# Optimization experiments

Measured on AMD Instinct MI355X. Metric: run time of the kernel, lower is better.

Reference implementation:

```python
import jax, jax.numpy as jnp
import numpy as np

B, CIN, COUT, H, W = 8, 256, 256, 64, 64
WBIT = 4  # weight_bit


def _fake_quant_sym(w, bits):
    # Symmetric per-tensor fake quantization with straight-through rounding.
    n = 2.0 ** (bits - 1) - 1
    mag = jax.lax.stop_gradient(
        jnp.maximum(jnp.abs(jnp.min(w)), jnp.abs(jnp.max(w))))
    s = jnp.maximum(mag, 1e-8) / n
    q = w / s
    q = q + jax.lax.stop_gradient(jnp.round(q) - q)  # STE round
    return jnp.clip(q, -n - 1, n) * s


def _conv3x3(x, w, b):
    out = jax.lax.conv_general_dilated(
        x, w, window_strides=(1, 1), padding=((1, 1), (1, 1)),
        dimension_numbers=('NCHW', 'OIHW', 'NCHW'))
    return out + b[None, :, None, None]


def _bilinear_gather(x, py, px):
    # x: [B,C,H,W]; py, px: [B,K,Ho,Wo] float sample coords. Zero outside.
    b, c, h, w = x.shape
    y0 = jnp.floor(py)
    x0 = jnp.floor(px)
    wy = (py - y0)[:, None]  # [B,1,K,Ho,Wo]
    wx = (px - x0)[:, None]
    flat = x.reshape(b, c, h * w)

    def gather(yi, xi):
        valid = (yi >= 0) & (yi <= h - 1) & (xi >= 0) & (xi <= w - 1)
        yc = jnp.clip(yi, 0, h - 1).astype(jnp.int32)
        xc = jnp.clip(xi, 0, w - 1).astype(jnp.int32)
        idx = (yc * w + xc).reshape(b, -1)  # [B, K*Ho*Wo]
        g = jax.vmap(lambda f, i: f[:, i])(flat, idx)  # [B,C,K*Ho*Wo]
        g = g.reshape(b, c, *yi.shape[1:])  # [B,C,K,Ho,Wo]
        return g * valid[:, None].astype(x.dtype)

    v00 = gather(y0, x0)
    v01 = gather(y0, x0 + 1)
    v10 = gather(y0 + 1, x0)
    v11 = gather(y0 + 1, x0 + 1)
    return (v00 * (1 - wy) * (1 - wx) + v01 * (1 - wy) * wx
            + v10 * wy * (1 - wx) + v11 * wy * wx)


def setup_inputs() -> dict:
    key = jax.random.key(0)
    ks = jax.random.split(key, 4)
    return {
        'x': jax.random.normal(ks[0], (B, CIN, H, W), jnp.float32),
        'w_off': jax.random.normal(ks[1], (2, CIN, 3, 3), jnp.float32) * 0.01,
        'b_off': jnp.zeros((2,), jnp.float32),
        'w_scale': jax.random.normal(ks[2], (1, CIN, 3, 3), jnp.float32) * 0.01,
        'b_scale': jnp.ones((1,), jnp.float32),
        'w_dcn': jax.random.normal(ks[3], (COUT, CIN, 3, 3), jnp.float32)
                 / np.float32(np.sqrt(CIN * 9)),
        'b_dcn': jnp.zeros((COUT,), jnp.float32),
    }


def reference(x, w_off, b_off, w_scale, b_scale, w_dcn, b_dcn):
    # Fake-quantize all conv weights (per-tensor symmetric, STE).
    w_off_q = _fake_quant_sym(w_off, WBIT)
    w_scale_q = _fake_quant_sym(w_scale, WBIT)
    w_dcn_q = _fake_quant_sym(w_dcn, WBIT)

    # Per-location offset (dy,dx) and positive-bounded scale.
    off = _conv3x3(x, w_off_q, b_off)                 # [B,2,H,W]
    scale = jax.nn.relu(_conv3x3(x, w_scale_q, b_scale))  # [B,1,H,W]

    # Kernel anchor grid (row-major 3x3, (ry,rx) in {-1,0,1}).
    ry = jnp.array([-1, -1, -1, 0, 0, 0, 1, 1, 1], jnp.float32)
    rx = jnp.array([-1, 0, 1, -1, 0, 1, -1, 0, 1], jnp.float32)
    ii = jnp.arange(H, dtype=jnp.float32)[None, None, :, None]
    jj = jnp.arange(W, dtype=jnp.float32)[None, None, None, :]
    # sample pos = base + anchor + [offset + anchor*(scale-1)] = base + anchor*scale + offset
    py = ii + ry[None, :, None, None] * scale + off[:, 0:1]   # [B,9,H,W]
    px = jj + rx[None, :, None, None] * scale + off[:, 1:2]

    sampled = _bilinear_gather(x, py, px)             # [B,C,9,H,W]
    out = jnp.einsum('bckhw,ock->bohw', sampled, w_dcn_q.reshape(COUT, CIN, 9))
    return out + b_dcn[None, :, None, None]
```

## Files before the change

kernel.cpp:

```cpp
#include <hip/hip_runtime.h>

#define BB   8
#define CIN  256
#define COUT 256
#define HH   64
#define WW   64
#define HW   (HH*WW)
#define KT   9
#define KTOT (CIN*KT)
#define NSLAB 16
#define WR   14
#define RSTR 65
#define CSTR 914

typedef short short8 __attribute__((ext_vector_type(8)));
typedef float f32x4  __attribute__((ext_vector_type(4)));
typedef float f32x2  __attribute__((ext_vector_type(2)));
union FragU { short8 s8; unsigned u[4]; uint4 u4; };

#define WS_OFF     0
#define WS_SCALE   65536
#define WS_PART    98304
#define WS_SDCN    98368
#define WS_WOFFQ   98372
#define WS_WSCALEQ 102980
#define WS_B       105284

#define USE_FP8_HW __has_builtin(__builtin_amdgcn_cvt_pk_f32_fp8)

__device__ __forceinline__ float fq(float w, float s) {
    float q = rintf(w / s);
    q = fminf(fmaxf(q, -8.f), 7.f);
    return q * s;
}

__device__ __forceinline__ unsigned short f2bf(float f) {
    unsigned u = __float_as_uint(f);
    return (unsigned short)((u + 0x7fffu + ((u >> 16) & 1u)) >> 16);
}

__global__ __launch_bounds__(256) void prep_kernel(const float* __restrict__ w_dcn,
                                                   const float* __restrict__ w_off,
                                                   const float* __restrict__ w_scale,
                                                   float* __restrict__ ws) {
    __shared__ float red[256];
    const int bx = blockIdx.x, tid = threadIdx.x;
    if (bx < 64) {
        float m = 0.f;
        const float* p = w_dcn + bx * 9216;
#pragma unroll
        for (int k = 0; k < 36; ++k) m = fmaxf(m, fabsf(p[tid + k * 256]));
        red[tid] = m;
        __syncthreads();
        for (int s = 128; s > 0; s >>= 1) {
            if (tid < s) red[tid] = fmaxf(red[tid], red[tid + s]);
            __syncthreads();
        }
        if (tid == 0) ws[WS_PART + bx] = red[0];
    } else {
        const float* src = (bx == 64) ? w_off : w_scale;
        const int n = (bx == 64) ? 2 * KTOT : KTOT;
        float* dst = ws + ((bx == 64) ? WS_WOFFQ : WS_WSCALEQ);
        float m = 0.f;
        for (int i = tid; i < n; i += 256) m = fmaxf(m, fabsf(src[i]));
        red[tid] = m;
        __syncthreads();
        for (int s = 128; s > 0; s >>= 1) {
            if (tid < s) red[tid] = fmaxf(red[tid], red[tid + s]);
            __syncthreads();
        }
        float sq = fmaxf(red[0], 1e-8f) / 7.f;
        for (int i = tid; i < n; i += 256) dst[i] = fq(src[i], sq);
    }
}

__global__ __launch_bounds__(256) void mid_kernel(const float* __restrict__ x,
                                                  const float* __restrict__ w_dcn,
                                                  float* __restrict__ ws) {
    __shared__ float R[4][3][64];
    const int bx = blockIdx.x, tid = threadIdx.x;
    if (bx < 512) {
        const int b = bx & 7, i = bx >> 3;
        const int j = tid & 63, cq = tid >> 6;
        const float* woq = ws + WS_WOFFQ;
        const float* wsq = ws + WS_WSCALEQ;
        float a0 = 0.f, a1 = 0.f, a2 = 0.f;
        for (int c = cq * 64; c < cq * 64 + 64; ++c) {
            const float* xb = x + (size_t)(b * CIN + c) * HW;
            const float* w0 = woq + c * 9;
            const float* w1 = woq + KTOT + c * 9;
            const float* w2 = wsq + c * 9;
#pragma unroll
            for (int di = -1; di <= 1; ++di) {
                int yy = i + di;
                bool rv = (yy >= 0) && (yy < HH);
#pragma unroll
                for (int dj = -1; dj <= 1; ++dj) {
                    int xx = j + dj;
                    float xv = (rv && xx >= 0 && xx < WW) ? xb[yy * WW + xx] : 0.f;
                    int t = (di + 1) * 3 + (dj + 1);
                    a0 += xv * w0[t];
                    a1 += xv * w1[t];
                    a2 += xv * w2[t];
                }
            }
        }
        R[cq][0][j] = a0; R[cq][1][j] = a1; R[cq][2][j] = a2;
        __syncthreads();
        if (tid < 192) {
            int comp = tid >> 6, j2 = tid & 63;
            float v = R[0][comp][j2] + R[1][comp][j2] +
                      R[2][comp][j2] + R[3][comp][j2];
            if (comp == 0)      ws[WS_OFF + (b * 2 + 0) * HW + i * WW + j2] = v;
            else if (comp == 1) ws[WS_OFF + (b * 2 + 1) * HW + i * WW + j2] = v;
            else                ws[WS_SCALE + b * HW + i * WW + j2] = v;
        }
    } else {
        const int qb = bx - 512;
        float m = 0.f;
#pragma unroll
        for (int k = 0; k < 64; ++k) m = fmaxf(m, ws[WS_PART + k]);
        float sd = fmaxf(m, 1e-8f) / 7.f;
        if (qb == 0 && tid == 0) ws[WS_SDCN] = sd;
        const int t4 = (qb * 256 + tid) * 4;
        float qv[4];
#pragma unroll
        for (int u = 0; u < 4; ++u) {
            int t = t4 + u;
            int j  = t & 7;
            int h  = (t >> 3) & 1;
            int l  = (t >> 4) & 63;
            int np = (t >> 10) & 7;
            int s  = t >> 13;
            int g = s / 5, p = s - g * 5;
            int k = ((l >> 4) << 3) + j;
            int ch = g * 16 + (k >> 1);
            int tap = p * 2 + (k & 1);
            int o = (np * 2 + h) * 16 + (l & 15);
            float w = (tap <= 8) ? w_dcn[(o * CIN + ch) * KT + tap] : 0.f;
            qv[u] = fminf(fmaxf(rintf(w / sd), -8.f), 7.f);
        }
        unsigned d;
#if USE_FP8_HW
        d = 0;
        d = __builtin_amdgcn_cvt_pk_fp8_f32(qv[0], qv[1], d, false);
        d = __builtin_amdgcn_cvt_pk_fp8_f32(qv[2], qv[3], d, true);
#else
        d = ((unsigned)(unsigned char)(signed char)(int)qv[0])
          | ((unsigned)(unsigned char)(signed char)(int)qv[1] << 8)
          | ((unsigned)(unsigned char)(signed char)(int)qv[2] << 16)
          | ((unsigned)(unsigned char)(signed char)(int)qv[3] << 24);
#endif
        ((unsigned*)(ws + WS_B))[qb * 256 + tid] = d;
    }
}

__device__ __forceinline__ void cvt4(unsigned d, unsigned& p0, unsigned& p1) {
#if USE_FP8_HW
    f32x2 lo = __builtin_amdgcn_cvt_pk_f32_fp8(d, false);
    f32x2 hi = __builtin_amdgcn_cvt_pk_f32_fp8(d, true);
    p0 = __builtin_amdgcn_perm(__float_as_uint(lo.y), __float_as_uint(lo.x),
                               0x07060302u);
    p1 = __builtin_amdgcn_perm(__float_as_uint(hi.y), __float_as_uint(hi.x),
                               0x07060302u);
#else
    float f0 = (float)(int)(signed char)(d & 0xff);
    float f1 = (float)(int)(signed char)((d >> 8) & 0xff);
    float f2 = (float)(int)(signed char)((d >> 16) & 0xff);
    float f3 = (float)(int)(signed char)(d >> 24);
    p0 = __builtin_amdgcn_perm(__float_as_uint(f1), __float_as_uint(f0),
                               0x07060302u);
    p1 = __builtin_amdgcn_perm(__float_as_uint(f3), __float_as_uint(f2),
                               0x07060302u);
#endif
}

__global__ __launch_bounds__(512, 2) void dcn_main_kernel(
    const float* __restrict__ x, const float* __restrict__ b_off,
    const float* __restrict__ b_scale, const float* __restrict__ b_dcn,
    const float* __restrict__ ws, float* __restrict__ out) {
    __shared__ unsigned sWin[2][16 * CSTR];
    __shared__ int sRed[2];
    const int tid = threadIdx.x;
    const int bx = blockIdx.x;
    const int b = bx & 7;
    const int i0 = (bx >> 3) * 2;
    const int w = tid >> 6, l = tid & 63;
    const int q = l >> 4, ln = l & 15;
    const int row_i = i0 + (w >> 2);
    const int colp = ((w & 3) << 4) + ln;
    const float* xb = x + (size_t)b * CIN * HW;
    const char* Bb = (const char*)(ws + WS_B);
    const float sdcn = ws[WS_SDCN];

    if (tid == 0) { sRed[0] = 64; sRed[1] = -1; }

    unsigned mRC[9], mW0[9], mW1[9];
    {
        float o0 = ws[WS_OFF + (b * 2 + 0) * HW + row_i * WW + colp] + b_off[0];
        float o1 = ws[WS_OFF + (b * 2 + 1) * HW + row_i * WW + colp] + b_off[1];
        float sc = fmaxf(ws[WS_SCALE + b * HW + row_i * WW + colp] + b_scale[0], 0.f);
        int rmn = 64, rmx = -1;
#pragma unroll
        for (int tap = 0; tap < 9; ++tap) {
            float ry = (float)(tap / 3 - 1), rx = (float)(tap % 3 - 1);
            float py = (float)row_i + ry * sc + o0;
            float px = (float)colp + rx * sc + o1;
            float y0f = floorf(py), x0f = floorf(px);
            float wy = py - y0f, wx = px - x0f;
            float w00 = (1.f - wy) * (1.f - wx), w01 = (1.f - wy) * wx;
            float w10 = wy * (1.f - wx),         w11 = wy * wx;
            bool vy0 = (y0f >= 0.f)  && (y0f <= 63.f);
            bool vy1 = (y0f >= -1.f) && (y0f <= 62.f);
            bool vx0 = (x0f >= 0.f)  && (x0f <= 63.f);
            bool vx1 = (x0f >= -1.f) && (x0f <= 62.f);
            bool d0hi = x0f > 62.f, d1lo = x0f < 0.f;
            float e0 = 0.f, e1 = 0.f, e2 = 0.f, e3 = 0.f;
            if (vy0 && vx0) { if (d0hi) e1 += w00; else e0 += w00; }
            if (vy0 && vx1) { if (d1lo) e0 += w01; else e1 += w01; }
            if (vy1 && vx0) { if (d0hi) e3 += w10; else e2 += w10; }
            if (vy1 && vx1) { if (d1lo) e2 += w11; else e3 += w11; }
            int r0 = (int)fminf(fmaxf(y0f, 0.f), 63.f);
            int r1 = (int)fminf(fmaxf(y0f + 1.f, 0.f), 63.f);
            int cb = (int)fminf(fmaxf(x0f, 0.f), 62.f);
            bool use0 = (e0 != 0.f) || (e1 != 0.f);
            bool use1 = (e2 != 0.f) || (e3 != 0.f);
            if (use0) { rmn = min(rmn, r0); rmx = max(rmx, r0); }
            if (use1) { rmn = min(rmn, r1); rmx = max(rmx, r1); }
            mRC[tap] = (unsigned)r0 | ((unsigned)r1 << 8) | ((unsigned)cb << 16) |
                       ((unsigned)use0 << 24) | ((unsigned)use1 << 25);
            mW0[tap] = (unsigned)f2bf(e0 * sdcn) | ((unsigned)f2bf(e1 * sdcn) << 16);
            mW1[tap] = (unsigned)f2bf(e2 * sdcn) | ((unsigned)f2bf(e3 * sdcn) << 16);
        }
        __syncthreads();
        atomicMin(&sRed[0], rmn);
        atomicMax(&sRed[1], rmx);
    }
    __syncthreads();
    const int rmin = sRed[0], rmax = sRed[1];
    const int rlo = min(max(rmin, 0), HH - WR);
    const bool fast = (rmax - rlo) <= (WR - 1);

    unsigned mOb[9];
#pragma unroll
    for (int tap = 0; tap < 9; ++tap) {
        unsigned rc = mRC[tap];
        int r0 = rc & 0xff, r1 = (rc >> 8) & 0xff, cb = (rc >> 16) & 0xff;
        int u0 = (rc >> 24) & 1, u1 = (rc >> 25) & 1;
        int a0, a1;
        if (fast) {
            a0 = ((u0 ? (r0 - rlo) : 0) * RSTR + cb) * 4;
            a1 = ((u1 ? (r1 - rlo) : 0) * RSTR + cb) * 4;
        } else {
            a0 = (r0 * WW + cb) * 4;
            a1 = (r1 * WW + cb) * 4;
        }
        mOb[tap] = (unsigned)a0 | ((unsigned)a1 << 16);
    }

    f32x4 acc[16];
#pragma unroll
    for (int n = 0; n < 16; ++n) acc[n] = (f32x4){0.f, 0.f, 0.f, 0.f};

    const char* winB = (const char*)&sWin[0][0] + q * 4 * (CSTR * 4);

    float4 stA[7]; float stB[7];
    auto stageLoad = [&](int g) {
#pragma unroll
        for (int sg = 0; sg < 7; ++sg) {
            int id = tid + sg * 512;
            int c4 = id & 15, rc = id >> 4;
            int ch = rc / WR, rr = rc - ch * WR;
            const float* src = xb + (size_t)(g * 16 + ch) * HW +
                               (rlo + rr) * WW + c4 * 4;
            stA[sg] = *(const float4*)src;
            stB[sg] = (c4 == 15) ? stA[sg].w : src[4];
        }
    };
    auto stageWrite = [&](int buf) {
#pragma unroll
        for (int sg = 0; sg < 7; ++sg) {
            int id = tid + sg * 512;
            int c4 = id & 15, rc = id >> 4;
            int ch = rc / WR, rr = rc - ch * WR;
            unsigned* wp = &sWin[buf][ch * CSTR + rr * RSTR + c4 * 4];
            float4 a = stA[sg]; float b5 = stB[sg];
            wp[0] = (unsigned)f2bf(a.x) | ((unsigned)f2bf(a.y) << 16);
            wp[1] = (unsigned)f2bf(a.y) | ((unsigned)f2bf(a.z) << 16);
            wp[2] = (unsigned)f2bf(a.z) | ((unsigned)f2bf(a.w) << 16);
            wp[3] = (unsigned)f2bf(a.w) | ((unsigned)f2bf(b5) << 16);
        }
    };

#define DECMFMA(RB, NP)                                                        \
    {                                                                          \
        FragU b0, b1;                                                          \
        cvt4(RB.x, b0.u[0], b0.u[1]); cvt4(RB.y, b0.u[2], b0.u[3]);            \
        cvt4(RB.z, b1.u[0], b1.u[1]); cvt4(RB.w, b1.u[2], b1.u[3]);            \
        acc[NP * 2 + 0] = __builtin_amdgcn_mfma_f32_16x16x32_bf16(             \
            af.s8, b0.s8, acc[NP * 2 + 0], 0, 0, 0);                           \
        acc[NP * 2 + 1] = __builtin_amdgcn_mfma_f32_16x16x32_bf16(             \
            af.s8, b1.s8, acc[NP * 2 + 1], 0, 0, 0);                           \
    }

#define KBODY(FASTMODE)                                                        \
    for (int g = 0; g < 16; ++g) {                                             \
        const int buf = g & 1;                                                 \
        if (FASTMODE && g < 15) stageLoad(g + 1);                              \
        _Pragma("unroll")                                                      \
        for (int p = 0; p < 5; ++p) {                                          \
            const int s = g * 5 + p;                                           \
            const char* bp = Bb + (size_t)s * 8192 + l * 16;                   \
            uint4 rb0 = *(const uint4*)(bp);                                   \
            uint4 rb1 = *(const uint4*)(bp + 1024);                            \
            uint4 rb2 = *(const uint4*)(bp + 2048);                            \
            uint4 rb3 = *(const uint4*)(bp + 3072);                            \
            uint4 rb4 = *(const uint4*)(bp + 4096);                            \
            uint4 rb5 = *(const uint4*)(bp + 5120);                            \
            uint4 rb6 = *(const uint4*)(bp + 6144);                            \
            uint4 rb7 = *(const uint4*)(bp + 7168);                            \
            FragU af;                                                          \
            _Pragma("unroll")                                                  \
            for (int jc = 0; jc < 4; ++jc) {                                   \
                float av0 = 0.f, av1 = 0.f;                                    \
                _Pragma("unroll")                                              \
                for (int t = 0; t < 2; ++t) {                                  \
                    const int tap = (2 * p + t > 8) ? 8 : (2 * p + t);         \
                    unsigned ob = mOb[tap];                                    \
                    float w00 = __uint_as_float(mW0[tap] << 16);               \
                    float w01 = __uint_as_float(mW0[tap] & 0xffff0000u);       \
                    float w10 = __uint_as_float(mW1[tap] << 16);               \
                    float w11 = __uint_as_float(mW1[tap] & 0xffff0000u);       \
                    float v;                                                   \
                    if (FASTMODE) {                                            \
                        const char* base = winB + buf * 58496 + jc * (CSTR * 4); \
                        unsigned dw0 = *(const unsigned*)(base + (ob & 0xffffu)); \
                        unsigned dw1 = *(const unsigned*)(base + (ob >> 16));  \
                        v = w00 * __uint_as_float(dw0 << 16) +                 \
                            w01 * __uint_as_float(dw0 & 0xffff0000u) +         \
                            w10 * __uint_as_float(dw1 << 16) +                 \
                            w11 * __uint_as_float(dw1 & 0xffff0000u);          \
                    } else {                                                   \
                        const char* pb = (const char*)(xb +                    \
                            (size_t)(g * 16 + q * 4 + jc) * HW);               \
                        float s0x = *(const float*)(pb + (ob & 0xffffu));      \
                        float s0y = *(const float*)(pb + (ob & 0xffffu) + 4);  \
                        float s1x = *(const float*)(pb + (ob >> 16));          \
                        float s1y = *(const float*)(pb + (ob >> 16) + 4);      \
                        v = w00 * s0x + w01 * s0y + w10 * s1x + w11 * s1y;     \
                    }                                                          \
                    if (t == 0) av0 = v; else av1 = v;                         \
                }                                                              \
                af.u[jc] = (unsigned)f2bf(av0) | ((unsigned)f2bf(av1) << 16);  \
            }                                                                  \
            DECMFMA(rb0, 0) DECMFMA(rb1, 1) DECMFMA(rb2, 2) DECMFMA(rb3, 3)    \
            DECMFMA(rb4, 4) DECMFMA(rb5, 5) DECMFMA(rb6, 6) DECMFMA(rb7, 7)    \
        }                                                                      \
        if (FASTMODE) {                                                        \
            if (g < 15) stageWrite(buf ^ 1);                                   \
            __syncthreads();                                                   \
        }                                                                      \
    }

    if (fast) {
        stageLoad(0);
        stageWrite(0);
        __syncthreads();
        KBODY(true)
    } else {
        KBODY(false)
    }
#undef KBODY
#undef DECMFMA

    const int col0 = ((w & 3) << 4) + (q << 2);
#pragma unroll
    for (int nt = 0; nt < 16; ++nt) {
        int o = nt * 16 + ln;
        float bb = b_dcn[o];
        f32x4 v = acc[nt];
        v.x += bb; v.y += bb; v.z += bb; v.w += bb;
        *(f32x4*)(out + ((size_t)(b * COUT + o) * HH + row_i) * WW + col0) = v;
    }
}

extern "C" void kernel_launch(void* const* d_in, const int* in_sizes, int n_in,
                              void* d_out, int out_size, void* d_ws, size_t ws_size,
                              hipStream_t stream) {
    const float* x       = (const float*)d_in[0];
    const float* w_off   = (const float*)d_in[1];
    const float* b_off   = (const float*)d_in[2];
    const float* w_scale = (const float*)d_in[3];
    const float* b_scale = (const float*)d_in[4];
    const float* w_dcn   = (const float*)d_in[5];
    const float* b_dcn   = (const float*)d_in[6];
    float* out = (float*)d_out;
    float* ws  = (float*)d_ws;

    prep_kernel<<<dim3(66),   dim3(256), 0, stream>>>(w_dcn, w_off, w_scale, ws);
    mid_kernel <<<dim3(1152), dim3(256), 0, stream>>>(x, w_dcn, ws);
    dcn_main_kernel<<<dim3(256), dim3(512), 0, stream>>>(
        x, b_off, b_scale, b_dcn, ws, out);
}
```

Measured before the change: 309.8 us.

## Restructure DCN main kernel to one row per block with shared A tiles and 32x32 MFMA

Each block now handles a single output row instead of two, so the grid grows from 256 to 512 blocks. The window buffer is single-buffered and smaller (12 rows) so occupancy can rise. Bilinear-sampled A fragments are built once per channel group into shared memory and reused by all waves. The MFMA shape moves from 16x16x32 to 32x32x16, with the quantized weight layout in prep rewritten to match. The intent is to stop every wave from resampling the same A data, cut weight-fragment traffic and raise occupancy, at the cost of extra barriers and reduced overlap between staging and compute.

```diff
diff --git a/kernel.cpp b/kernel.cpp
--- a/kernel.cpp
+++ b/kernel.cpp
@@ -8,14 +8,14 @@
 #define HW   (HH*WW)
 #define KT   9
 #define KTOT (CIN*KT)
-#define NSLAB 16
-#define WR   14
+#define WR   12
 #define RSTR 65
-#define CSTR 914
+#define CSTR 786
 
 typedef short short8 __attribute__((ext_vector_type(8)));
 typedef float f32x4  __attribute__((ext_vector_type(4)));
 typedef float f32x2  __attribute__((ext_vector_type(2)));
+typedef float f32x16 __attribute__((ext_vector_type(16)));
 union FragU { short8 s8; unsigned u[4]; uint4 u4; };
 
 #define WS_OFF     0
@@ -128,15 +128,14 @@
         for (int u = 0; u < 4; ++u) {
             int t = t4 + u;
             int j  = t & 7;
-            int h  = (t >> 3) & 1;
-            int l  = (t >> 4) & 63;
-            int np = (t >> 10) & 7;
-            int s  = t >> 13;
-            int g = s / 5, p = s - g * 5;
-            int k = ((l >> 4) << 3) + j;
-            int ch = g * 16 + (k >> 1);
-            int tap = p * 2 + (k & 1);
-            int o = (np * 2 + h) * 16 + (l & 15);
+            int l  = (t >> 3) & 63;
+            int nt = (t >> 9) & 7;
+            int s  = t >> 12;
+            int g = s / 10, r = s - g * 10;
+            int p = r >> 1, o8 = r & 1;
+            int ch = g * 16 + o8 * 8 + ((l >> 5) << 2) + (j >> 1);
+            int tap = 2 * p + (j & 1);
+            int o = nt * 32 + (l & 31);
             float w = (tap <= 8) ? w_dcn[(o * CIN + ch) * KT + tap] : 0.f;
             qv[u] = fminf(fmaxf(rintf(w / sd), -8.f), 7.f);
         }
@@ -175,20 +174,22 @@
 #endif
 }
 
-__global__ __launch_bounds__(512, 2) void dcn_main_kernel(
+__global__ __launch_bounds__(512, 4) void dcn_main_kernel(
     const float* __restrict__ x, const float* __restrict__ b_off,
     const float* __restrict__ b_scale, const float* __restrict__ b_dcn,
     const float* __restrict__ ws, float* __restrict__ out) {
-    __shared__ unsigned sWin[2][16 * CSTR];
+    __shared__ unsigned sWin[16 * CSTR];
+    __shared__ short8 sA[10][2][64];
     __shared__ int sRed[2];
     const int tid = threadIdx.x;
     const int bx = blockIdx.x;
     const int b = bx & 7;
-    const int i0 = (bx >> 3) * 2;
+    const int i = bx >> 3;
     const int w = tid >> 6, l = tid & 63;
-    const int q = l >> 4, ln = l & 15;
-    const int row_i = i0 + (w >> 2);
-    const int colp = ((w & 3) << 4) + ln;
+    const int h = l >> 5;
+    const int mtp = w & 1;
+    const int colp = mtp * 32 + (l & 31);
+    const int mtc = w & 1, ntp = w >> 1;
     const float* xb = x + (size_t)b * CIN * HW;
     const char* Bb = (const char*)(ws + WS_B);
     const float sdcn = ws[WS_SDCN];
@@ -197,14 +198,14 @@
 
     unsigned mRC[9], mW0[9], mW1[9];
     {
-        float o0 = ws[WS_OFF + (b * 2 + 0) * HW + row_i * WW + colp] + b_off[0];
-        float o1 = ws[WS_OFF + (b * 2 + 1) * HW + row_i * WW + colp] + b_off[1];
-        float sc = fmaxf(ws[WS_SCALE + b * HW + row_i * WW + colp] + b_scale[0], 0.f);
+        float o0 = ws[WS_OFF + (b * 2 + 0) * HW + i * WW + colp] + b_off[0];
+        float o1 = ws[WS_OFF + (b * 2 + 1) * HW + i * WW + colp] + b_off[1];
+        float sc = fmaxf(ws[WS_SCALE + b * HW + i * WW + colp] + b_scale[0], 0.f);
         int rmn = 64, rmx = -1;
 #pragma unroll
         for (int tap = 0; tap < 9; ++tap) {
             float ry = (float)(tap / 3 - 1), rx = (float)(tap % 3 - 1);
-            float py = (float)row_i + ry * sc + o0;
+            float py = (float)i + ry * sc + o0;
             float px = (float)colp + rx * sc + o1;
             float y0f = floorf(py), x0f = floorf(px);
             float wy = py - y0f, wx = px - x0f;
@@ -258,33 +259,89 @@
         mOb[tap] = (unsigned)a0 | ((unsigned)a1 << 16);
     }
 
-    f32x4 acc[16];
-#pragma unroll
-    for (int n = 0; n < 16; ++n) acc[n] = (f32x4){0.f, 0.f, 0.f, 0.f};
-
-    const char* winB = (const char*)&sWin[0][0] + q * 4 * (CSTR * 4);
-
-    float4 stA[7]; float stB[7];
-    auto stageLoad = [&](int g) {
-#pragma unroll
-        for (int sg = 0; sg < 7; ++sg) {
-            int id = tid + sg * 512;
-            int c4 = id & 15, rc = id >> 4;
-            int ch = rc / WR, rr = rc - ch * WR;
+    f32x16 acc0 = {0.f}, acc1 = {0.f};
+#pragma unroll
+    for (int r = 0; r < 16; ++r) { acc0[r] = 0.f; acc1[r] = 0.f; }
+
+    auto produceUnit = [&](int g, int ksl, bool fastm) {
+        const int p = ksl >> 1, o8 = ksl & 1;
+        FragU af;
+#pragma unroll
+        for (int jc = 0; jc < 4; ++jc) {
+            float vv0 = 0.f, vv1 = 0.f;
+            const int chs = o8 * 8 + h * 4 + jc;
+#pragma unroll
+            for (int t = 0; t < 2; ++t) {
+                int tap = 2 * p + t; if (tap > 8) tap = 8;
+                unsigned ob = mOb[tap];
+                float w00 = __uint_as_float(mW0[tap] << 16);
+                float w01 = __uint_as_float(mW0[tap] & 0xffff0000u);
+                float w10 = __uint_as_float(mW1[tap] << 16);
+                float w11 = __uint_as_float(mW1[tap] & 0xffff0000u);
+                float v;
+                if (fastm) {
+                    const char* base = (const char*)sWin + chs * (CSTR * 4);
+                    unsigned dw0 = *(const unsigned*)(base + (ob & 0xffffu));
+                    unsigned dw1 = *(const unsigned*)(base + (ob >> 16));
+                    v = w00 * __uint_as_float(dw0 << 16) +
+                        w01 * __uint_as_float(dw0 & 0xffff0000u) +
+                        w10 * __uint_as_float(dw1 << 16) +
+                        w11 * __uint_as_float(dw1 & 0xffff0000u);
+                } else {
+                    const char* pb = (const char*)(xb + (size_t)(g * 16 + chs) * HW);
+                    float s0x = *(const float*)(pb + (ob & 0xffffu));
+                    float s0y = *(const float*)(pb + (ob & 0xffffu) + 4);
+                    float s1x = *(const float*)(pb + (ob >> 16));
+                    float s1y = *(const float*)(pb + (ob >> 16) + 4);
+                    v = w00 * s0x + w01 * s0y + w10 * s1x + w11 * s1y;
+                }
+                if (t == 0) vv0 = v; else vv1 = v;
+            }
+            af.u[jc] = (unsigned)f2bf(vv0) | ((unsigned)f2bf(vv1) << 16);
+        }
+        sA[ksl][mtp][l] = af.s8;
+    };
+    auto produceAll = [&](int g, bool fastm) {
+        produceUnit(g, w >> 1, fastm);
+        produceUnit(g, (w + 8) >> 1, fastm);
+        if (w < 4) produceUnit(g, (w + 16) >> 1, fastm);
+    };
+
+    auto consumeStep = [&](int g, int ks) {
+        const int s = g * 10 + ks;
+        short8 af = sA[ks][mtc][l];
+        const char* bp = Bb + ((size_t)(s * 8 + ntp * 2) * 64 + l) * 8;
+        uint2 r0 = *(const uint2*)bp;
+        uint2 r1 = *(const uint2*)(bp + 512);
+        FragU b0, b1;
+        cvt4(r0.x, b0.u[0], b0.u[1]); cvt4(r0.y, b0.u[2], b0.u[3]);
+        cvt4(r1.x, b1.u[0], b1.u[1]); cvt4(r1.y, b1.u[2], b1.u[3]);
+        acc0 = __builtin_amdgcn_mfma_f32_32x32x16_bf16(af, b0.s8, acc0, 0, 0, 0);
+        acc1 = __builtin_amdgcn_mfma_f32_32x32x16_bf16(af, b1.s8, acc1, 0, 0, 0);
+    };
+
+    const int c4 = tid & 15;
+    float4 sa[3]; float sb[3];
+    auto stageLoad3 = [&](int g, int c0) {
+#pragma unroll
+        for (int c = 0; c < 3; ++c) {
+            int id = tid + (c0 + c) * 512;
+            int rowIdx = id >> 4;
+            int ch = rowIdx / WR, rr = rowIdx - ch * WR;
             const float* src = xb + (size_t)(g * 16 + ch) * HW +
                                (rlo + rr) * WW + c4 * 4;
-            stA[sg] = *(const float4*)src;
-            stB[sg] = (c4 == 15) ? stA[sg].w : src[4];
+            sa[c] = *(const float4*)src;
+            sb[c] = (c4 == 15) ? sa[c].w : src[4];
         }
     };
-    auto stageWrite = [&](int buf) {
-#pragma unroll
-        for (int sg = 0; sg < 7; ++sg) {
-            int id = tid + sg * 512;
-            int c4 = id & 15, rc = id >> 4;
-            int ch = rc / WR, rr = rc - ch * WR;
-            unsigned* wp = &sWin[buf][ch * CSTR + rr * RSTR + c4 * 4];
-            float4 a = stA[sg]; float b5 = stB[sg];
+    auto stageWrite3 = [&](int c0) {
+#pragma unroll
+        for (int c = 0; c < 3; ++c) {
+            int id = tid + (c0 + c) * 512;
+            int rowIdx = id >> 4;
+            int ch = rowIdx / WR, rr = rowIdx - ch * WR;
+            unsigned* wp = &sWin[ch * CSTR + rr * RSTR + c4 * 4];
+            float4 a = sa[c]; float b5 = sb[c];
             wp[0] = (unsigned)f2bf(a.x) | ((unsigned)f2bf(a.y) << 16);
             wp[1] = (unsigned)f2bf(a.y) | ((unsigned)f2bf(a.z) << 16);
             wp[2] = (unsigned)f2bf(a.z) | ((unsigned)f2bf(a.w) << 16);
@@ -292,95 +349,49 @@
         }
     };
 
-#define DECMFMA(RB, NP)                                                        \
-    {                                                                          \
-        FragU b0, b1;                                                          \
-        cvt4(RB.x, b0.u[0], b0.u[1]); cvt4(RB.y, b0.u[2], b0.u[3]);            \
-        cvt4(RB.z, b1.u[0], b1.u[1]); cvt4(RB.w, b1.u[2], b1.u[3]);            \
-        acc[NP * 2 + 0] = __builtin_amdgcn_mfma_f32_16x16x32_bf16(             \
-            af.s8, b0.s8, acc[NP * 2 + 0], 0, 0, 0);                           \
-        acc[NP * 2 + 1] = __builtin_amdgcn_mfma_f32_16x16x32_bf16(             \
-            af.s8, b1.s8, acc[NP * 2 + 1], 0, 0, 0);                           \
-    }
-
-#define KBODY(FASTMODE)                                                        \
-    for (int g = 0; g < 16; ++g) {                                             \
-        const int buf = g & 1;                                                 \
-        if (FASTMODE && g < 15) stageLoad(g + 1);                              \
-        _Pragma("unroll")                                                      \
-        for (int p = 0; p < 5; ++p) {                                          \
-            const int s = g * 5 + p;                                           \
-            const char* bp = Bb + (size_t)s * 8192 + l * 16;                   \
-            uint4 rb0 = *(const uint4*)(bp);                                   \
-            uint4 rb1 = *(const uint4*)(bp + 1024);                            \
-            uint4 rb2 = *(const uint4*)(bp + 2048);                            \
-            uint4 rb3 = *(const uint4*)(bp + 3072);                            \
-            uint4 rb4 = *(const uint4*)(bp + 4096);                            \
-            uint4 rb5 = *(const uint4*)(bp + 5120);                            \
-            uint4 rb6 = *(const uint4*)(bp + 6144);                            \
-            uint4 rb7 = *(const uint4*)(bp + 7168);                            \
-            FragU af;                                                          \
-            _Pragma("unroll")                                                  \
-            for (int jc = 0; jc < 4; ++jc) {                                   \
-                float av0 = 0.f, av1 = 0.f;                                    \
-                _Pragma("unroll")                                              \
-                for (int t = 0; t < 2; ++t) {                                  \
-                    const int tap = (2 * p + t > 8) ? 8 : (2 * p + t);         \
-                    unsigned ob = mOb[tap];                                    \
-                    float w00 = __uint_as_float(mW0[tap] << 16);               \
-                    float w01 = __uint_as_float(mW0[tap] & 0xffff0000u);       \
-                    float w10 = __uint_as_float(mW1[tap] << 16);               \
-                    float w11 = __uint_as_float(mW1[tap] & 0xffff0000u);       \
-                    float v;                                                   \
-                    if (FASTMODE) {                                            \
-                        const char* base = winB + buf * 58496 + jc * (CSTR * 4); \
-                        unsigned dw0 = *(const unsigned*)(base + (ob & 0xffffu)); \
-                        unsigned dw1 = *(const unsigned*)(base + (ob >> 16));  \
-                        v = w00 * __uint_as_float(dw0 << 16) +                 \
-                            w01 * __uint_as_float(dw0 & 0xffff0000u) +         \
-                            w10 * __uint_as_float(dw1 << 16) +                 \
-                            w11 * __uint_as_float(dw1 & 0xffff0000u);          \
-                    } else {                                                   \
-                        const char* pb = (const char*)(xb +                    \
-                            (size_t)(g * 16 + q * 4 + jc) * HW);               \
-                        float s0x = *(const float*)(pb + (ob & 0xffffu));      \
-                        float s0y = *(const float*)(pb + (ob & 0xffffu) + 4);  \
-                        float s1x = *(const float*)(pb + (ob >> 16));          \
-                        float s1y = *(const float*)(pb + (ob >> 16) + 4);      \
-                        v = w00 * s0x + w01 * s0y + w10 * s1x + w11 * s1y;     \
-                    }                                                          \
-                    if (t == 0) av0 = v; else av1 = v;                         \
-                }                                                              \
-                af.u[jc] = (unsigned)f2bf(av0) | ((unsigned)f2bf(av1) << 16);  \
-            }                                                                  \
-            DECMFMA(rb0, 0) DECMFMA(rb1, 1) DECMFMA(rb2, 2) DECMFMA(rb3, 3)    \
-            DECMFMA(rb4, 4) DECMFMA(rb5, 5) DECMFMA(rb6, 6) DECMFMA(rb7, 7)    \
-        }                                                                      \
-        if (FASTMODE) {                                                        \
-            if (g < 15) stageWrite(buf ^ 1);                                   \
-            __syncthreads();                                                   \
-        }                                                                      \
-    }
-
     if (fast) {
-        stageLoad(0);
-        stageWrite(0);
-        __syncthreads();
-        KBODY(true)
+        stageLoad3(0, 0); stageWrite3(0);
+        stageLoad3(0, 3); stageWrite3(3);
+        __syncthreads();
+        produceAll(0, true);
+        __syncthreads();
+        for (int g = 0; g < 16; ++g) {
+            const bool hn = g < 15;
+            if (hn) stageLoad3(g + 1, 0);
+            consumeStep(g, 0); consumeStep(g, 1); consumeStep(g, 2);
+            consumeStep(g, 3); consumeStep(g, 4);
+            if (hn) { stageWrite3(0); stageLoad3(g + 1, 3); }
+            consumeStep(g, 5); consumeStep(g, 6); consumeStep(g, 7);
+            consumeStep(g, 8); consumeStep(g, 9);
+            if (hn) stageWrite3(3);
+            __syncthreads();
+            if (hn) {
+                produceAll(g + 1, true);
+                __syncthreads();
+            }
+        }
     } else {
-        KBODY(false)
-    }
-#undef KBODY
-#undef DECMFMA
-
-    const int col0 = ((w & 3) << 4) + (q << 2);
-#pragma unroll
-    for (int nt = 0; nt < 16; ++nt) {
-        int o = nt * 16 + ln;
+        for (int g = 0; g < 16; ++g) {
+            produceAll(g, false);
+            __syncthreads();
+#pragma unroll
+            for (int ks = 0; ks < 10; ++ks) consumeStep(g, ks);
+            __syncthreads();
+        }
+    }
+
+#pragma unroll
+    for (int t = 0; t < 2; ++t) {
+        f32x16 A = t ? acc1 : acc0;
+        int o = (ntp * 2 + t) * 32 + (l & 31);
         float bb = b_dcn[o];
-        f32x4 v = acc[nt];
-        v.x += bb; v.y += bb; v.z += bb; v.w += bb;
-        *(f32x4*)(out + ((size_t)(b * COUT + o) * HH + row_i) * WW + col0) = v;
+        float* ob = out + ((size_t)(b * COUT + o) * HH + i) * WW + mtc * 32 + 4 * h;
+#pragma unroll
+        for (int rq = 0; rq < 4; ++rq) {
+            f32x4 v = {A[rq * 4 + 0] + bb, A[rq * 4 + 1] + bb,
+                       A[rq * 4 + 2] + bb, A[rq * 4 + 3] + bb};
+            *(f32x4*)(ob + rq * 8) = v;
+        }
     }
 }
 
@@ -399,6 +410,6 @@
 
     prep_kernel<<<dim3(66),   dim3(256), 0, stream>>>(w_dcn, w_off, w_scale, ws);
     mid_kernel <<<dim3(1152), dim3(256), 0, stream>>>(x, w_dcn, ws);
-    dcn_main_kernel<<<dim3(256), dim3(512), 0, stream>>>(
+    dcn_main_kernel<<<dim3(512), dim3(512), 0, stream>>>(
         x, b_off, b_scale, b_dcn, ws, out);
 }
```

Result: faster. 285.7 us (-7.8%).
